# Optimization experiments

Hardware: AMD Instinct MI355X
Metric: run time of the kernel (lower is better)

## Reference

```python
import jax, jax.numpy as jnp
import numpy as np

D_MODEL = 1024
N_HEADS = 16
HEAD_DIM = D_MODEL // N_HEADS
D_FF = 4096
BATCH = 4
SEQ = 2048
LN_EPS = 1e-5


def layer_norm(x, g, b):
    mu = jnp.mean(x, axis=-1, keepdims=True)
    var = jnp.mean(jnp.square(x - mu), axis=-1, keepdims=True)
    return (x - mu) * jax.lax.rsqrt(var + LN_EPS) * g + b


def setup_inputs() -> dict:
    key = jax.random.key(0)
    ks = jax.random.split(key, 8)
    s = 0.02
    x = jax.random.normal(ks[0], (BATCH, SEQ, D_MODEL), jnp.float32)
    mask = jnp.triu(jnp.ones((SEQ, SEQ), dtype=bool), k=1)  # True = masked
    return {
        "x": x,
        "ln1_g": jnp.ones((D_MODEL,), jnp.float32),
        "ln1_b": jnp.zeros((D_MODEL,), jnp.float32),
        "qkv_w": jax.random.normal(ks[1], (3 * D_MODEL, D_MODEL), jnp.float32) * s,
        "qkv_b": jnp.zeros((3 * D_MODEL,), jnp.float32),
        "out_w": jax.random.normal(ks[2], (D_MODEL, D_MODEL), jnp.float32) * s,
        "out_b": jnp.zeros((D_MODEL,), jnp.float32),
        "ln2_g": jnp.ones((D_MODEL,), jnp.float32),
        "ln2_b": jnp.zeros((D_MODEL,), jnp.float32),
        "fc1_w": jax.random.normal(ks[3], (D_FF, D_MODEL), jnp.float32) * s,
        "fc1_b": jnp.zeros((D_FF,), jnp.float32),
        "fc2_w": jax.random.normal(ks[4], (D_MODEL, D_FF), jnp.float32) * s,
        "fc2_b": jnp.zeros((D_MODEL,), jnp.float32),
        "mask": mask,
    }


def reference(x, ln1_g, ln1_b, qkv_w, qkv_b, out_w, out_b,
              ln2_g, ln2_b, fc1_w, fc1_b, fc2_w, fc2_b, mask):
    b, s, _ = x.shape
    # --- pre-norm attention ---
    h = layer_norm(x, ln1_g, ln1_b)
    qkv = h @ qkv_w.T + qkv_b                       # [b, s, 3*D]
    qkv = qkv.reshape(b, s, 3, N_HEADS, HEAD_DIM)
    q, k, v = (jnp.moveaxis(qkv[:, :, i], 2, 1) for i in range(3))  # [b, H, s, hd]
    scale = HEAD_DIM ** -0.5
    attn = jnp.einsum('bhqd,bhkd->bhqk', q, k) * scale
    attn = jnp.where(mask, -jnp.inf, attn)
    attn = jax.nn.softmax(attn, axis=-1)
    o = jnp.einsum('bhqk,bhkd->bhqd', attn, v)      # [b, H, s, hd]
    o = jnp.moveaxis(o, 1, 2).reshape(b, s, D_MODEL)
    x = x + (o @ out_w.T + out_b)
    # --- pre-norm FFN ---
    h = layer_norm(x, ln2_g, ln2_b)
    h = jax.nn.gelu(h @ fc1_w.T + fc1_b, approximate=False)
    x = x + (h @ fc2_w.T + fc2_b)
    return x
```

## Files before the change

### kernel.cpp

```cpp
#include <hip/hip_runtime.h>
#include <math.h>

using u16 = unsigned short;
typedef __attribute__((ext_vector_type(8))) short short8;
typedef __attribute__((ext_vector_type(4))) float f32x4;
typedef __attribute__((ext_vector_type(16))) float f32x16;
typedef __attribute__((ext_vector_type(4))) u16 u16x4;

#define DEV __device__ __forceinline__

DEV u16 f2bf(float f) {
    unsigned u = __float_as_uint(f);
    u += 0x7fffu + ((u >> 16) & 1u);
    return (u16)(u >> 16);
}
DEV float bf2f(u16 h) { return __uint_as_float(((unsigned)h) << 16); }

DEV short8 ld16(const u16* p) { return *reinterpret_cast<const short8*>(p); }

DEV float gelu_f(float x) { return 0.5f * x * (1.f + erff(x * 0.70710678118654752f)); }

DEV unsigned pk2(float a, float b) {
    unsigned r;
    asm("v_cvt_pk_bf16_f32 %0, %1, %2" : "=v"(r) : "v"(a), "v"(b));
    return r;
}

#define GLL16(gp, lp)                                                          \
    __builtin_amdgcn_global_load_lds(                                          \
        (const __attribute__((address_space(1))) void*)(gp),                   \
        (__attribute__((address_space(3))) void*)(lp), 16, 0, 0)

#define VMC(n) asm volatile("s_waitcnt vmcnt(" #n ")" ::: "memory")
#define LGKM0() asm volatile("s_waitcnt lgkmcnt(0)" ::: "memory")

__global__ void cvt_f32_bf16(const float* __restrict__ in, u16* __restrict__ out, int n4) {
    int i = blockIdx.x * 256 + threadIdx.x;
    if (i >= n4) return;
    float4 v = reinterpret_cast<const float4*>(in)[i];
    u16x4 o;
    o.x = f2bf(v.x); o.y = f2bf(v.y); o.z = f2bf(v.z); o.w = f2bf(v.w);
    reinterpret_cast<u16x4*>(out)[i] = o;
}

__global__ __launch_bounds__(256) void ln_bf16(const float* __restrict__ x,
                                               const float* __restrict__ gm,
                                               const float* __restrict__ bt,
                                               u16* __restrict__ out) {
    const int row = blockIdx.x, tid = threadIdx.x;
    const float4 v = reinterpret_cast<const float4*>(x + (long)row * 1024)[tid];
    float s  = v.x + v.y + v.z + v.w;
    float sq = v.x * v.x + v.y * v.y + v.z * v.z + v.w * v.w;
#pragma unroll
    for (int off = 1; off <= 32; off <<= 1) {
        s  += __shfl_xor(s, off);
        sq += __shfl_xor(sq, off);
    }
    __shared__ float ss[4], ssq[4];
    const int wave = tid >> 6, lane = tid & 63;
    if (lane == 0) { ss[wave] = s; ssq[wave] = sq; }
    __syncthreads();
    s  = ss[0] + ss[1] + ss[2] + ss[3];
    sq = ssq[0] + ssq[1] + ssq[2] + ssq[3];
    const float mu   = s * (1.f / 1024.f);
    const float var  = sq * (1.f / 1024.f) - mu * mu;
    const float rstd = rsqrtf(var + 1e-5f);
    const float4 g4 = reinterpret_cast<const float4*>(gm)[tid];
    const float4 b4 = reinterpret_cast<const float4*>(bt)[tid];
    u16x4 o;
    o.x = f2bf((v.x - mu) * rstd * g4.x + b4.x);
    o.y = f2bf((v.y - mu) * rstd * g4.y + b4.y);
    o.z = f2bf((v.z - mu) * rstd * g4.z + b4.z);
    o.w = f2bf((v.w - mu) * rstd * g4.w + b4.w);
    reinterpret_cast<u16x4*>(out + (long)row * 1024)[tid] = o;
}

#define TS(c, r) ((c) * 128 + (((((r) >> 3) ^ ((c) & 15))) << 3) + ((r) & 7))

template <int EPI>
__global__ __launch_bounds__(256, 3) void gemm_bt(
    const u16* __restrict__ A, const u16* __restrict__ B,
    const float* __restrict__ bias, const float* res, float* outf,
    u16* __restrict__ outb, u16* __restrict__ Qb, u16* __restrict__ Kb,
    u16* __restrict__ Vtb, int M, int N, int K) {
    __shared__ u16 shpool[16384];

    const int tid = threadIdx.x;
    const int wave = tid >> 6, lane = tid & 63;
    const int lo = lane & 15, g = lane >> 4;
    const int wr = wave >> 1, wc = wave & 1;

    const int nwg = gridDim.x, chunk = nwg >> 3;
    const int wgid = (blockIdx.x & 7) * chunk + (blockIdx.x >> 3);
    const int NB = N >> 7;
    const int bm = wgid / NB, bn = wgid % NB;
    const int row0 = bm * 128, col0 = bn * 128;

    const int lrow = lane >> 2;
    const int lg   = (lane & 3) ^ ((lane >> 3) & 3);
    const u16* Ag = A + (long)(row0 + wave * 16 + lrow) * K + lg * 8;
    const u16* Bg = B + (long)(col0 + wave * 16 + lrow) * K + lg * 8;

#define STAGE(tb, kt) do {                                                     \
        u16* Al = shpool + (tb) * 8192 + wave * 512;                           \
        u16* Bl = Al + 4096;                                                   \
        GLL16(Ag + (long)(kt) * 32, Al);                                       \
        GLL16(Ag + 64 * (long)K + (long)(kt) * 32, Al + 2048);                 \
        GLL16(Bg + (long)(kt) * 32, Bl);                                       \
        GLL16(Bg + 64 * (long)K + (long)(kt) * 32, Bl + 2048);                 \
    } while (0)

    const int agp = g ^ ((lo >> 1) & 3);
    f32x4 acc[4][4] = {};

    STAGE(0, 0);
    STAGE(1, 1);

    const int T = K >> 5;
    for (int t = 0; t < T; ++t) {
        const int cur = t & 1;
        if (t + 2 < T) { VMC(4); } else { VMC(0); }
        __builtin_amdgcn_s_barrier();
        const u16* As = shpool + cur * 8192;
        const u16* Bs = As + 4096;
        short8 af[4], bfr[4];
#pragma unroll
        for (int m = 0; m < 4; ++m)
            af[m] = ld16(&As[(wr * 64 + m * 16 + lo) * 32 + agp * 8]);
#pragma unroll
        for (int n = 0; n < 4; ++n)
            bfr[n] = ld16(&Bs[(wc * 64 + n * 16 + lo) * 32 + agp * 8]);
        LGKM0();
        __builtin_amdgcn_s_barrier();
        if (t + 2 < T) STAGE(cur, t + 2);
#pragma unroll
        for (int m = 0; m < 4; ++m)
#pragma unroll
            for (int n = 0; n < 4; ++n)
                acc[m][n] = __builtin_amdgcn_mfma_f32_16x16x32_bf16(
                    bfr[n], af[m], acc[m][n], 0, 0, 0);
    }
#undef STAGE

    if constexpr (EPI == 3) {
        if (col0 >= 2048) {
            __syncthreads();
#pragma unroll
            for (int n = 0; n < 4; ++n) {
                const int cb = wc * 64 + n * 16 + g * 4;
                const float4 b4 = *reinterpret_cast<const float4*>(&bias[col0 + cb]);
#pragma unroll
                for (int m = 0; m < 4; ++m) {
                    const int rl = wr * 64 + m * 16 + lo;
                    shpool[TS(cb + 0, rl)] = f2bf(acc[m][n][0] + b4.x);
                    shpool[TS(cb + 1, rl)] = f2bf(acc[m][n][1] + b4.y);
                    shpool[TS(cb + 2, rl)] = f2bf(acc[m][n][2] + b4.z);
                    shpool[TS(cb + 3, rl)] = f2bf(acc[m][n][3] + b4.w);
                }
            }
            __syncthreads();
            const int c = tid >> 1, half = tid & 1;
            const int dcol = (col0 - 2048) + c;
            const int head = dcol >> 6, d = dcol & 63;
            const int bb = row0 >> 11;
            u16* dst = Vtb + ((long)(bb * 16 + head) * 64 + d) * 2048 +
                       (row0 & 2047) + half * 64;
            const u16* srcb = shpool + c * 128;
#pragma unroll
            for (int i = 0; i < 8; ++i) {
                const int pc = (half * 8 + i) ^ (c & 15);
                *reinterpret_cast<short8*>(dst + i * 8) =
                    *reinterpret_cast<const short8*>(srcb + pc * 8);
            }
            return;
        }
    }
#pragma unroll
    for (int n = 0; n < 4; ++n) {
        const int cb = col0 + wc * 64 + n * 16 + g * 4;
        const float4 b4 = *reinterpret_cast<const float4*>(&bias[cb]);
#pragma unroll
        for (int m = 0; m < 4; ++m) {
            const int r = row0 + wr * 64 + m * 16 + lo;
            const float v0 = acc[m][n][0] + b4.x;
            const float v1 = acc[m][n][1] + b4.y;
            const float v2 = acc[m][n][2] + b4.z;
            const float v3 = acc[m][n][3] + b4.w;
            if constexpr (EPI == 0) {
                u16x4 o = {f2bf(v0), f2bf(v1), f2bf(v2), f2bf(v3)};
                *reinterpret_cast<u16x4*>(&outb[(long)r * N + cb]) = o;
            } else if constexpr (EPI == 1) {
                u16x4 o = {f2bf(gelu_f(v0)), f2bf(gelu_f(v1)),
                           f2bf(gelu_f(v2)), f2bf(gelu_f(v3))};
                *reinterpret_cast<u16x4*>(&outb[(long)r * N + cb]) = o;
            } else if constexpr (EPI == 2) {
                const float4 rr = *reinterpret_cast<const float4*>(&res[(long)r * N + cb]);
                float4 o = {rr.x + v0, rr.y + v1, rr.z + v2, rr.w + v3};
                *reinterpret_cast<float4*>(&outf[(long)r * N + cb]) = o;
            } else {
                const int part = cb >> 10, cc = cb & 1023;
                const int head = cc >> 6, d = cc & 63;
                const int bb = r >> 11, srow = r & 2047;
                const int bh = bb * 16 + head;
                const float qs = (part == 0) ? 0.18033688f : 1.0f;
                u16x4 o = {f2bf(v0 * qs), f2bf(v1 * qs), f2bf(v2 * qs), f2bf(v3 * qs)};
                u16* base = (part == 0) ? Qb : Kb;
                *reinterpret_cast<u16x4*>(&base[((long)bh * 2048 + srow) * 64 + d]) = o;
            }
        }
    }
}

__global__ __launch_bounds__(256) void attn_fwd32(
    const u16* __restrict__ Q, const u16* __restrict__ K,
    const u16* __restrict__ Vt, u16* __restrict__ O) {
    const int wave = threadIdx.x >> 6, lane = threadIdx.x & 63;
    const int job = blockIdx.x * 4 + wave;
    const int qt = 63 - (job >> 6);
    const int bh = job & 63;
    const int lq = lane & 31, hi = lane >> 5;
    const int qw = qt * 32;

    const u16* Kp = K + (long)bh * 2048 * 64;
    const u16* Vp = Vt + (long)bh * 64 * 2048;
    const int bb = bh >> 4, h = bh & 15;
    const u16* Qp = Q + ((long)bh * 2048 + qw) * 64;

    short8 qf[4];
#pragma unroll
    for (int ks = 0; ks < 4; ++ks)
        qf[ks] = ld16(Qp + lq * 64 + ks * 16 + hi * 8);

    f32x16 o0 = {}, o1 = {};
    float m = -1e30f, l = 0.f;
    const int q_abs = qw + lq;
    const int nkv = qw + 32;

    for (int kv0 = 0; kv0 < nkv; kv0 += 64) {
        f32x16 s0 = {}, s1 = {};
        const u16* Kr = Kp + (long)(kv0 + lq) * 64 + hi * 8;
        __builtin_amdgcn_s_setprio(1);
#pragma unroll
        for (int ks = 0; ks < 4; ++ks)
            s0 = __builtin_amdgcn_mfma_f32_32x32x16_bf16(
                ld16(Kr + ks * 16), qf[ks], s0, 0, 0, 0);
        const u16* Kr2 = Kr + 32 * 64;
#pragma unroll
        for (int ks = 0; ks < 4; ++ks)
            s1 = __builtin_amdgcn_mfma_f32_32x32x16_bf16(
                ld16(Kr2 + ks * 16), qf[ks], s1, 0, 0, 0);
        __builtin_amdgcn_s_setprio(0);

        const u16* Vr = Vp + (long)lq * 2048 + kv0 + hi * 8;
        short8 vf0[4], vf1[4];
#pragma unroll
        for (int c = 0; c < 4; ++c) {
            vf0[c] = ld16(Vr + c * 16);
            vf1[c] = ld16(Vr + 32 * 2048 + c * 16);
        }

        float mt = -1e30f;
        if (kv0 + 64 >= nkv) {
#pragma unroll
            for (int r = 0; r < 16; ++r) {
                const int kv = kv0 + (r & 3) + 8 * (r >> 2) + 4 * hi;
                if (kv > q_abs) s0[r] = -1e30f;
                mt = fmaxf(mt, s0[r]);
                if (kv + 32 > q_abs) s1[r] = -1e30f;
                mt = fmaxf(mt, s1[r]);
            }
        } else {
#pragma unroll
            for (int r = 0; r < 16; ++r)
                mt = fmaxf(mt, fmaxf(s0[r], s1[r]));
        }
        mt = fmaxf(mt, __shfl_xor(mt, 32));

        if (!__all(mt <= m + 11.5f)) {
            const float mn = fmaxf(m, mt);
            const float corr = __builtin_amdgcn_exp2f(m - mn);
            m = mn;
            l *= corr;
            o0 *= corr; o1 *= corr;
        }
        float ps = 0.f;
#pragma unroll
        for (int r = 0; r < 16; ++r) {
            s0[r] = __builtin_amdgcn_exp2f(s0[r] - m); ps += s0[r];
            s1[r] = __builtin_amdgcn_exp2f(s1[r] - m); ps += s1[r];
        }
        l += ps;

        short8 pf[4];
#pragma unroll
        for (int c = 0; c < 4; ++c) {
            const f32x16& src = (c >> 1) ? s1 : s0;
            const int b = (c & 1) * 8;
            const unsigned A0 = pk2(src[b + 0], src[b + 1]);
            const unsigned A1 = pk2(src[b + 2], src[b + 3]);
            const unsigned B0 = pk2(src[b + 4], src[b + 5]);
            const unsigned B1 = pk2(src[b + 6], src[b + 7]);
            const unsigned S0 = hi ? A0 : B0;
            const unsigned S1 = hi ? A1 : B1;
            const unsigned R0 = (unsigned)__shfl_xor((int)S0, 32);
            const unsigned R1 = (unsigned)__shfl_xor((int)S1, 32);
            union { unsigned u[4]; short8 v; } fr;
            fr.u[0] = hi ? R0 : A0;
            fr.u[1] = hi ? R1 : A1;
            fr.u[2] = hi ? B0 : R0;
            fr.u[3] = hi ? B1 : R1;
            pf[c] = fr.v;
        }

        __builtin_amdgcn_s_setprio(1);
#pragma unroll
        for (int c = 0; c < 4; ++c) {
            o0 = __builtin_amdgcn_mfma_f32_32x32x16_bf16(
                vf0[c], pf[c], o0, 0, 0, 0);
            o1 = __builtin_amdgcn_mfma_f32_32x32x16_bf16(
                vf1[c], pf[c], o1, 0, 0, 0);
        }
        __builtin_amdgcn_s_setprio(0);
    }

    l += __shfl_xor(l, 32);
    const float inv = 1.f / l;
    u16* Orow = O + ((long)(bb * 2048 + qw + lq)) * 1024 + h * 64;
#pragma unroll
    for (int k4 = 0; k4 < 4; ++k4) {
        u16x4 w0, w1;
#pragma unroll
        for (int j = 0; j < 4; ++j) {
            w0[j] = f2bf(o0[k4 * 4 + j] * inv);
            w1[j] = f2bf(o1[k4 * 4 + j] * inv);
        }
        *reinterpret_cast<u16x4*>(Orow + 8 * k4 + 4 * hi)      = w0;
        *reinterpret_cast<u16x4*>(Orow + 32 + 8 * k4 + 4 * hi) = w1;
    }
}

extern "C" void kernel_launch(void* const* d_in, const int* in_sizes, int n_in,
                              void* d_out, int out_size, void* d_ws, size_t ws_size,
                              hipStream_t stream) {
    const float* x      = (const float*)d_in[0];
    const float* ln1_g  = (const float*)d_in[1];
    const float* ln1_b  = (const float*)d_in[2];
    const float* qkv_w  = (const float*)d_in[3];
    const float* qkv_b  = (const float*)d_in[4];
    const float* out_w  = (const float*)d_in[5];
    const float* out_b  = (const float*)d_in[6];
    const float* ln2_g  = (const float*)d_in[7];
    const float* ln2_b  = (const float*)d_in[8];
    const float* fc1_w  = (const float*)d_in[9];
    const float* fc1_b  = (const float*)d_in[10];
    const float* fc2_w  = (const float*)d_in[11];
    const float* fc2_b  = (const float*)d_in[12];
    float* out = (float*)d_out;

    const size_t MB = 1024ull * 1024ull;
    if (ws_size < 120 * MB) return;
    char* ws = (char*)d_ws;
    u16* wqkv = (u16*)(ws + 0);
    u16* wout = (u16*)(ws + 6 * MB);
    u16* wfc1 = (u16*)(ws + 8 * MB);
    u16* wfc2 = (u16*)(ws + 16 * MB);
    u16* hbuf = (u16*)(ws + 24 * MB);
    u16* obuf = (u16*)(ws + 40 * MB);
    u16* Qb   = (u16*)(ws + 56 * MB);
    u16* Kb   = (u16*)(ws + 72 * MB);
    u16* Vtb  = (u16*)(ws + 88 * MB);
    u16* gbuf = (u16*)(ws + 56 * MB);

    cvt_f32_bf16<<<3072, 256, 0, stream>>>(qkv_w, wqkv, 3072 * 1024 / 4);
    cvt_f32_bf16<<<1024, 256, 0, stream>>>(out_w, wout, 1024 * 1024 / 4);
    cvt_f32_bf16<<<4096, 256, 0, stream>>>(fc1_w, wfc1, 4096 * 1024 / 4);
    cvt_f32_bf16<<<4096, 256, 0, stream>>>(fc2_w, wfc2, 1024 * 4096 / 4);

    ln_bf16<<<8192, 256, 0, stream>>>(x, ln1_g, ln1_b, hbuf);
    gemm_bt<3><<<dim3(1536), 256, 0, stream>>>(hbuf, wqkv, qkv_b, nullptr,
                                               nullptr, nullptr, Qb, Kb, Vtb,
                                               8192, 3072, 1024);
    attn_fwd32<<<dim3(1024), 256, 0, stream>>>(Qb, Kb, Vtb, obuf);
    gemm_bt<2><<<dim3(512), 256, 0, stream>>>(obuf, wout, out_b, x, out,
                                              nullptr, nullptr, nullptr, nullptr,
                                              8192, 1024, 1024);
    ln_bf16<<<8192, 256, 0, stream>>>(out, ln2_g, ln2_b, hbuf);
    gemm_bt<1><<<dim3(2048), 256, 0, stream>>>(hbuf, wfc1, fc1_b, nullptr,
                                               nullptr, gbuf, nullptr, nullptr,
                                               nullptr, 8192, 4096, 1024);
    gemm_bt<2><<<dim3(512), 256, 0, stream>>>(gbuf, wfc2, fc2_b, out, out,
                                              nullptr, nullptr, nullptr, nullptr,
                                              8192, 1024, 4096);
}
```

Measured before the change: 445.8 us.

## Share K/V tiles in LDS across attention waves and triple-buffer GEMM stages

```diff
diff --git a/kernel.cpp b/kernel.cpp
--- a/kernel.cpp
+++ b/kernel.cpp
@@ -83,7 +83,7 @@
     const float* __restrict__ bias, const float* res, float* outf,
     u16* __restrict__ outb, u16* __restrict__ Qb, u16* __restrict__ Kb,
     u16* __restrict__ Vtb, int M, int N, int K) {
-    __shared__ u16 shpool[16384];
+    __shared__ u16 shpool[24576];
 
     const int tid = threadIdx.x;
     const int wave = tid >> 6, lane = tid & 63;
@@ -115,11 +115,14 @@
 
     STAGE(0, 0);
     STAGE(1, 1);
+    STAGE(2, 2);
 
     const int T = K >> 5;
+    int cur = 0;
     for (int t = 0; t < T; ++t) {
-        const int cur = t & 1;
-        if (t + 2 < T) { VMC(4); } else { VMC(0); }
+        if (t + 2 < T) { VMC(8); }
+        else if (t + 1 < T) { VMC(4); }
+        else { VMC(0); }
         __builtin_amdgcn_s_barrier();
         const u16* As = shpool + cur * 8192;
         const u16* Bs = As + 4096;
@@ -132,13 +135,14 @@
             bfr[n] = ld16(&Bs[(wc * 64 + n * 16 + lo) * 32 + agp * 8]);
         LGKM0();
         __builtin_amdgcn_s_barrier();
-        if (t + 2 < T) STAGE(cur, t + 2);
+        if (t + 3 < T) STAGE(cur, t + 3);
 #pragma unroll
         for (int m = 0; m < 4; ++m)
 #pragma unroll
             for (int n = 0; n < 4; ++n)
                 acc[m][n] = __builtin_amdgcn_mfma_f32_16x16x32_bf16(
                     bfr[n], af[m], acc[m][n], 0, 0, 0);
+        cur = (cur == 2) ? 0 : cur + 1;
     }
 #undef STAGE
 
@@ -214,17 +218,29 @@
 __global__ __launch_bounds__(256) void attn_fwd32(
     const u16* __restrict__ Q, const u16* __restrict__ K,
     const u16* __restrict__ Vt, u16* __restrict__ O) {
+    __shared__ u16 kvl[2][8192];
+    const int bh = blockIdx.x;
+    const int strip = 15 - blockIdx.y;
     const int wave = threadIdx.x >> 6, lane = threadIdx.x & 63;
-    const int job = blockIdx.x * 4 + wave;
-    const int qt = 63 - (job >> 6);
-    const int bh = job & 63;
     const int lq = lane & 31, hi = lane >> 5;
-    const int qw = qt * 32;
-
-    const u16* Kp = K + (long)bh * 2048 * 64;
-    const u16* Vp = Vt + (long)bh * 64 * 2048;
+    const int qw = strip * 128 + wave * 32;
+
+    const u16* Kg = K + (long)bh * 2048 * 64;
+    const u16* Vg = Vt + (long)bh * 64 * 2048;
     const int bb = bh >> 4, h = bh & 15;
     const u16* Qp = Q + ((long)bh * 2048 + qw) * 64;
+
+    const int srow = wave * 8 + (lane >> 3);
+    const int sc   = (lane & 7) ^ (srow & 7);
+
+#define ASTAGE(b, kt) do {                                                     \
+        const long kvb = (long)(kt) * 64;                                      \
+        GLL16(Kg + (kvb + srow) * 64 + sc * 8,        &kvl[b][wave * 512]);    \
+        GLL16(Kg + (kvb + 32 + srow) * 64 + sc * 8,   &kvl[b][2048 + wave * 512]); \
+        GLL16(Vg + (long)srow * 2048 + kvb + sc * 8,  &kvl[b][4096 + wave * 512]); \
+        GLL16(Vg + (long)(32 + srow) * 2048 + kvb + sc * 8,                    \
+              &kvl[b][6144 + wave * 512]);                                     \
+    } while (0)
 
     short8 qf[4];
 #pragma unroll
@@ -234,94 +250,109 @@
     f32x16 o0 = {}, o1 = {};
     float m = -1e30f, l = 0.f;
     const int q_abs = qw + lq;
-    const int nkv = qw + 32;
-
-    for (int kv0 = 0; kv0 < nkv; kv0 += 64) {
+    const int my_end = qw + 32;
+    const int T = 2 * (strip + 1);
+    const int swp = lq & 7;
+
+    ASTAGE(0, 0);
+    ASTAGE(1, 1);
+
+    for (int t = 0; t < T; ++t) {
+        const int cur = t & 1;
+        const int kv0 = t * 64;
+        if (t + 1 < T) { VMC(4); } else { VMC(0); }
+        __builtin_amdgcn_s_barrier();
+        const bool active = (kv0 < my_end);
         f32x16 s0 = {}, s1 = {};
-        const u16* Kr = Kp + (long)(kv0 + lq) * 64 + hi * 8;
-        __builtin_amdgcn_s_setprio(1);
-#pragma unroll
-        for (int ks = 0; ks < 4; ++ks)
-            s0 = __builtin_amdgcn_mfma_f32_32x32x16_bf16(
-                ld16(Kr + ks * 16), qf[ks], s0, 0, 0, 0);
-        const u16* Kr2 = Kr + 32 * 64;
-#pragma unroll
-        for (int ks = 0; ks < 4; ++ks)
-            s1 = __builtin_amdgcn_mfma_f32_32x32x16_bf16(
-                ld16(Kr2 + ks * 16), qf[ks], s1, 0, 0, 0);
-        __builtin_amdgcn_s_setprio(0);
-
-        const u16* Vr = Vp + (long)lq * 2048 + kv0 + hi * 8;
         short8 vf0[4], vf1[4];
-#pragma unroll
-        for (int c = 0; c < 4; ++c) {
-            vf0[c] = ld16(Vr + c * 16);
-            vf1[c] = ld16(Vr + 32 * 2048 + c * 16);
+        if (active) {
+            const u16* Kb = &kvl[cur][0];
+            __builtin_amdgcn_s_setprio(1);
+#pragma unroll
+            for (int ks = 0; ks < 4; ++ks)
+                s0 = __builtin_amdgcn_mfma_f32_32x32x16_bf16(
+                    ld16(Kb + lq * 64 + ((ks * 2 + hi) ^ swp) * 8), qf[ks], s0, 0, 0, 0);
+#pragma unroll
+            for (int ks = 0; ks < 4; ++ks)
+                s1 = __builtin_amdgcn_mfma_f32_32x32x16_bf16(
+                    ld16(Kb + 2048 + lq * 64 + ((ks * 2 + hi) ^ swp) * 8), qf[ks], s1, 0, 0, 0);
+            __builtin_amdgcn_s_setprio(0);
+            const u16* Vb = &kvl[cur][4096];
+#pragma unroll
+            for (int c = 0; c < 4; ++c) {
+                vf0[c] = ld16(Vb + lq * 64 + ((c * 2 + hi) ^ swp) * 8);
+                vf1[c] = ld16(Vb + 2048 + lq * 64 + ((c * 2 + hi) ^ swp) * 8);
+            }
         }
-
-        float mt = -1e30f;
-        if (kv0 + 64 >= nkv) {
+        LGKM0();
+        __builtin_amdgcn_s_barrier();
+        if (t + 2 < T) ASTAGE(cur, t + 2);
+        if (active) {
+            float mt = -1e30f;
+            if (kv0 + 64 >= my_end) {
+#pragma unroll
+                for (int r = 0; r < 16; ++r) {
+                    const int kv = kv0 + (r & 3) + 8 * (r >> 2) + 4 * hi;
+                    if (kv > q_abs) s0[r] = -1e30f;
+                    mt = fmaxf(mt, s0[r]);
+                    if (kv + 32 > q_abs) s1[r] = -1e30f;
+                    mt = fmaxf(mt, s1[r]);
+                }
+            } else {
+#pragma unroll
+                for (int r = 0; r < 16; ++r)
+                    mt = fmaxf(mt, fmaxf(s0[r], s1[r]));
+            }
+            mt = fmaxf(mt, __shfl_xor(mt, 32));
+
+            if (!__all(mt <= m + 11.5f)) {
+                const float mn = fmaxf(m, mt);
+                const float corr = __builtin_amdgcn_exp2f(m - mn);
+                m = mn;
+                l *= corr;
+                o0 *= corr; o1 *= corr;
+            }
+            float ps = 0.f;
 #pragma unroll
             for (int r = 0; r < 16; ++r) {
-                const int kv = kv0 + (r & 3) + 8 * (r >> 2) + 4 * hi;
-                if (kv > q_abs) s0[r] = -1e30f;
-                mt = fmaxf(mt, s0[r]);
-                if (kv + 32 > q_abs) s1[r] = -1e30f;
-                mt = fmaxf(mt, s1[r]);
-            }
-        } else {
-#pragma unroll
-            for (int r = 0; r < 16; ++r)
-                mt = fmaxf(mt, fmaxf(s0[r], s1[r]));
+                s0[r] = __builtin_amdgcn_exp2f(s0[r] - m); ps += s0[r];
+                s1[r] = __builtin_amdgcn_exp2f(s1[r] - m); ps += s1[r];
+            }
+            l += ps;
+
+            short8 pf[4];
+#pragma unroll
+            for (int c = 0; c < 4; ++c) {
+                const f32x16& src = (c >> 1) ? s1 : s0;
+                const int b = (c & 1) * 8;
+                const unsigned A0 = pk2(src[b + 0], src[b + 1]);
+                const unsigned A1 = pk2(src[b + 2], src[b + 3]);
+                const unsigned B0 = pk2(src[b + 4], src[b + 5]);
+                const unsigned B1 = pk2(src[b + 6], src[b + 7]);
+                const unsigned S0 = hi ? A0 : B0;
+                const unsigned S1 = hi ? A1 : B1;
+                const unsigned R0 = (unsigned)__shfl_xor((int)S0, 32);
+                const unsigned R1 = (unsigned)__shfl_xor((int)S1, 32);
+                union { unsigned u[4]; short8 v; } fr;
+                fr.u[0] = hi ? R0 : A0;
+                fr.u[1] = hi ? R1 : A1;
+                fr.u[2] = hi ? B0 : R0;
+                fr.u[3] = hi ? B1 : R1;
+                pf[c] = fr.v;
+            }
+
+            __builtin_amdgcn_s_setprio(1);
+#pragma unroll
+            for (int c = 0; c < 4; ++c) {
+                o0 = __builtin_amdgcn_mfma_f32_32x32x16_bf16(
+                    vf0[c], pf[c], o0, 0, 0, 0);
+                o1 = __builtin_amdgcn_mfma_f32_32x32x16_bf16(
+                    vf1[c], pf[c], o1, 0, 0, 0);
+            }
+            __builtin_amdgcn_s_setprio(0);
         }
-        mt = fmaxf(mt, __shfl_xor(mt, 32));
-
-        if (!__all(mt <= m + 11.5f)) {
-            const float mn = fmaxf(m, mt);
-            const float corr = __builtin_amdgcn_exp2f(m - mn);
-            m = mn;
-            l *= corr;
-            o0 *= corr; o1 *= corr;
-        }
-        float ps = 0.f;
-#pragma unroll
-        for (int r = 0; r < 16; ++r) {
-            s0[r] = __builtin_amdgcn_exp2f(s0[r] - m); ps += s0[r];
-            s1[r] = __builtin_amdgcn_exp2f(s1[r] - m); ps += s1[r];
-        }
-        l += ps;
-
-        short8 pf[4];
-#pragma unroll
-        for (int c = 0; c < 4; ++c) {
-            const f32x16& src = (c >> 1) ? s1 : s0;
-            const int b = (c & 1) * 8;
-            const unsigned A0 = pk2(src[b + 0], src[b + 1]);
-            const unsigned A1 = pk2(src[b + 2], src[b + 3]);
-            const unsigned B0 = pk2(src[b + 4], src[b + 5]);
-            const unsigned B1 = pk2(src[b + 6], src[b + 7]);
-            const unsigned S0 = hi ? A0 : B0;
-            const unsigned S1 = hi ? A1 : B1;
-            const unsigned R0 = (unsigned)__shfl_xor((int)S0, 32);
-            const unsigned R1 = (unsigned)__shfl_xor((int)S1, 32);
-            union { unsigned u[4]; short8 v; } fr;
-            fr.u[0] = hi ? R0 : A0;
-            fr.u[1] = hi ? R1 : A1;
-            fr.u[2] = hi ? B0 : R0;
-            fr.u[3] = hi ? B1 : R1;
-            pf[c] = fr.v;
-        }
-
-        __builtin_amdgcn_s_setprio(1);
-#pragma unroll
-        for (int c = 0; c < 4; ++c) {
-            o0 = __builtin_amdgcn_mfma_f32_32x32x16_bf16(
-                vf0[c], pf[c], o0, 0, 0, 0);
-            o1 = __builtin_amdgcn_mfma_f32_32x32x16_bf16(
-                vf1[c], pf[c], o1, 0, 0, 0);
-        }
-        __builtin_amdgcn_s_setprio(0);
-    }
+    }
+#undef ASTAGE
 
     l += __shfl_xor(l, 32);
     const float inv = 1.f / l;
@@ -380,7 +411,7 @@
     gemm_bt<3><<<dim3(1536), 256, 0, stream>>>(hbuf, wqkv, qkv_b, nullptr,
                                                nullptr, nullptr, Qb, Kb, Vtb,
                                                8192, 3072, 1024);
-    attn_fwd32<<<dim3(1024), 256, 0, stream>>>(Qb, Kb, Vtb, obuf);
+    attn_fwd32<<<dim3(64, 16), 256, 0, stream>>>(Qb, Kb, Vtb, obuf);
     gemm_bt<2><<<dim3(512), 256, 0, stream>>>(obuf, wout, out_b, x, out,
                                               nullptr, nullptr, nullptr, nullptr,
                                               8192, 1024, 1024);
```

Measured after the change: 404.6 us. -9.2%, faster.
